# Kernel tuning notes

Measured on AMD Instinct MI355X. Metric: run time of the kernel, lower is better.

Reference implementation:

```python
import jax, jax.numpy as jnp
import numpy as np

HEADS = 4

def _topk_mask(attn, k):
    # exact replica of mask.scatter_(-1, topk_indices, 1.0): exactly k ones per row
    C = attn.shape[-1]
    _, idx = jax.lax.top_k(attn, k)                      # [b,h,C,k]
    return jax.nn.one_hot(idx, C, dtype=attn.dtype).sum(axis=-2) > 0  # [b,h,C,C] bool


def setup_inputs() -> dict:
    key = jax.random.key(0)
    ks = jax.random.split(key, 8)
    b, dim, h, w = 32, 128, 4096, 1
    s = 0.05
    return {
        "x": jax.random.normal(ks[0], (b, dim, h, w), jnp.float32),
        "qkv_w": jax.random.normal(ks[1], (3 * dim, dim), jnp.float32) * s,
        "qkv_b": jax.random.normal(ks[2], (3 * dim,), jnp.float32) * s,
        "dw_w": jax.random.normal(ks[3], (3 * dim, 1, 3, 3), jnp.float32) * s,
        "dw_b": jax.random.normal(ks[4], (3 * dim,), jnp.float32) * s,
        "proj_w": jax.random.normal(ks[5], (dim, dim), jnp.float32) * s,
        "proj_b": jax.random.normal(ks[6], (dim,), jnp.float32) * s,
        "temperature": jnp.ones((HEADS, 1, 1), jnp.float32),
        "attn_w": jnp.full((4,), 0.2, jnp.float32),  # attn1..attn4
    }


def reference(x, qkv_w, qkv_b, dw_w, dw_b, proj_w, proj_b, temperature, attn_w):
    b, c, h, w = x.shape
    # 1x1 conv qkv, then 3x3 depthwise conv (groups = 3*c)
    qkv = jnp.einsum('bchw,oc->bohw', x, qkv_w) + qkv_b[None, :, None, None]
    qkv = jax.lax.conv_general_dilated(
        qkv, dw_w, window_strides=(1, 1), padding=((1, 1), (1, 1)),
        dimension_numbers=('NCHW', 'OIHW', 'NCHW'), feature_group_count=3 * c
    ) + dw_b[None, :, None, None]
    q, k, v = jnp.split(qkv, 3, axis=1)
    heads = lambda t: t.reshape(b, HEADS, c // HEADS, h * w)  # b head c (hw)
    q, k, v = heads(q), heads(k), heads(v)
    # F.normalize(dim=-1), eps=1e-12
    q = q / jnp.maximum(jnp.linalg.norm(q, axis=-1, keepdims=True), 1e-12)
    k = k / jnp.maximum(jnp.linalg.norm(k, axis=-1, keepdims=True), 1e-12)
    C = c // HEADS
    attn = jnp.einsum('bhcn,bhdn->bhcd', q, k) * temperature[None]  # [b,head,C,C]
    top_ks = [C // 2, (2 * C) // 3, (3 * C) // 4, (4 * C) // 5]
    out = jnp.zeros_like(v)
    for i, kk in enumerate(top_ks):
        m = _topk_mask(attn, kk)
        a = jax.nn.softmax(jnp.where(m, attn, -jnp.inf), axis=-1)
        out = out + attn_w[i] * jnp.einsum('bhcd,bhdn->bhcn', a, v)
    out = out.reshape(b, c, h, w)
    out = jnp.einsum('bchw,oc->bohw', out, proj_w) + proj_b[None, :, None, None]
    return out
```

## Files before the change

kernel.cpp:

```cpp
#include <hip/hip_runtime.h>

#define B_ 32
#define CD 128
#define O3 384
#define N  4096
#define H_ 4
#define C_ 32

typedef __bf16 bf16x8 __attribute__((ext_vector_type(8)));
typedef float floatx4 __attribute__((ext_vector_type(4)));

#define MFMA16(a, b, c) __builtin_amdgcn_mfma_f32_16x16x32_bf16(a, b, c, 0, 0, 0)

__device__ __forceinline__ float b2f(unsigned int u) {
  return __builtin_bit_cast(float, u << 16);
}
__device__ __forceinline__ float b2fh(unsigned int u) {
  return __builtin_bit_cast(float, u & 0xffff0000u);
}
__device__ __forceinline__ unsigned short f2b(float f) {
  unsigned int bits = __builtin_bit_cast(unsigned int, f);
  unsigned int r = (bits + 0x7FFFu + ((bits >> 16) & 1u)) >> 16;
  return (unsigned short)r;
}

__global__ __launch_bounds__(256) void k0_xt(const float* __restrict__ x,
                                             unsigned short* __restrict__ xT)
{
  __shared__ float xt[32 * 66];
  const int t = threadIdx.x;
  const int n0 = blockIdx.x * 64, c0 = blockIdx.y * 32, b = blockIdx.z;
  const float* xb = x + ((size_t)b * CD + c0) * N + n0;
#pragma unroll
  for (int i = 0; i < 2; i++) {
    int f = i * 256 + t;
    int c = f >> 4, n4 = (f & 15) * 4;
    float4 v = *(const float4*)(xb + (size_t)c * N + n4);
    *(float2*)&xt[c * 66 + n4]     = make_float2(v.x, v.y);
    *(float2*)&xt[c * 66 + n4 + 2] = make_float2(v.z, v.w);
  }
  __syncthreads();
  int n = t >> 2, cb = (t & 3) * 8;
  unsigned short tmp[8];
#pragma unroll
  for (int j = 0; j < 8; j++) tmp[j] = f2b(xt[(cb + j) * 66 + n]);
  *(uint4*)(xT + ((size_t)b * N + n0 + n) * CD + c0 + cb) = *(uint4*)tmp;
}

__global__ void k0_w(const float* __restrict__ qkv_w,
                     const float* __restrict__ proj_w,
                     const float* __restrict__ dw_w,
                     const float* __restrict__ dw_b,
                     unsigned short* __restrict__ qkv_wb,
                     unsigned short* __restrict__ proj_wb,
                     float4* __restrict__ dwq)
{
  int e = (blockIdx.x * 256 + threadIdx.x) * 4;
  if (e < 49152) {
    float4 v = *(const float4*)(qkv_w + e);
    unsigned short tmp[4] = {f2b(v.x), f2b(v.y), f2b(v.z), f2b(v.w)};
    *(uint2*)(qkv_wb + e) = *(uint2*)tmp;
  } else if (e < 65536) {
    int off = e - 49152;
    float4 v = *(const float4*)(proj_w + off);
    unsigned short tmp[4] = {f2b(v.x), f2b(v.y), f2b(v.z), f2b(v.w)};
    *(uint2*)(proj_wb + off) = *(uint2*)tmp;
  } else {
    int o = (e - 65536) >> 2;
    if (o < 384)
      dwq[o] = make_float4(dw_w[o * 9 + 1], dw_w[o * 9 + 4],
                           dw_w[o * 9 + 7], dw_b[o]);
  }
}

__global__ __launch_bounds__(256, 4) void k1_qkv_dw(
    const unsigned short* __restrict__ xT, const unsigned short* __restrict__ qkv_wb,
    const float* __restrict__ qkv_b, const float4* __restrict__ dwq,
    unsigned short* __restrict__ qkvd, unsigned short* __restrict__ vT)
{
  __shared__ __align__(16) char smem[34816];
  unsigned short* Bs   = (unsigned short*)smem;
  unsigned short* pres = (unsigned short*)smem;

  const int t = threadIdx.x;
  const int otile = blockIdx.x, ytile = blockIdx.y, b = blockIdx.z;
  const int obase = otile * 128;
  const int ybase = ytile * 124;
  const int wv = t >> 6, l = t & 63, quad = l >> 4, lm = l & 15;

  const unsigned short* wbase =
      qkv_wb + (size_t)(obase + wv * 32 + lm) * CD + quad * 8;
  bf16x8 wa0[4], wa1[4];
#pragma unroll
  for (int ks = 0; ks < 4; ks++) {
    wa0[ks] = *(const bf16x8*)(wbase + ks * 32);
    wa1[ks] = *(const bf16x8*)(wbase + 16 * CD + ks * 32);
  }

  if (ytile >= 1 && ytile <= 32) {
#pragma unroll
    for (int i = 0; i < 8; i++) {
      int f = i * 256 + t;
      int row = f >> 4, c8 = (f & 15) * 8;
      *(uint4*)&Bs[row * 136 + c8] =
          *(const uint4*)(xT + ((size_t)b * N + ybase - 2 + row) * CD + c8);
    }
  } else {
#pragma unroll
    for (int i = 0; i < 8; i++) {
      int f = i * 256 + t;
      int row = f >> 4, c8 = (f & 15) * 8;
      int yg = ybase - 2 + row;
      uint4 v = make_uint4(0u, 0u, 0u, 0u);
      if (yg >= 0 && yg < N)
        v = *(const uint4*)(xT + ((size_t)b * N + yg) * CD + c8);
      *(uint4*)&Bs[row * 136 + c8] = v;
    }
  }
  __syncthreads();

  floatx4 acc[2][8];
#pragma unroll
  for (int mt = 0; mt < 2; mt++)
#pragma unroll
    for (int nt = 0; nt < 8; nt++) acc[mt][nt] = (floatx4){0.f, 0.f, 0.f, 0.f};

#pragma unroll
  for (int ks = 0; ks < 4; ks++) {
#pragma unroll
    for (int nt = 0; nt < 8; nt++) {
      bf16x8 bb = *(const bf16x8*)&Bs[(nt * 16 + lm) * 136 + ks * 32 + quad * 8];
      acc[0][nt] = MFMA16(wa0[ks], bb, acc[0][nt]);
      acc[1][nt] = MFMA16(wa1[ks], bb, acc[1][nt]);
    }
  }

  if (otile < 2) {
    __syncthreads();
#pragma unroll
    for (int mt = 0; mt < 2; mt++)
#pragma unroll
      for (int r = 0; r < 4; r++) {
        int o = wv * 32 + mt * 16 + quad * 4 + r;
        float bias = qkv_b[obase + o];
#pragma unroll
        for (int nt = 0; nt < 8; nt++) {
          int i = nt * 16 + lm;
          if (i >= 1) {
            int yg = ybase - 2 + i;
            pres[o * 132 + (i - 1)] =
                f2b((yg >= 0 && yg < N) ? (acc[mt][nt][r] + bias) : 0.f);
          }
        }
      }
    __syncthreads();
    const int p = t & 63, og = t >> 6;
    const bool ok = (p < 62) && (ybase + 2 * p < N);
    const unsigned int* presu = (const unsigned int*)pres;
    for (int r2 = 0; r2 < 32; r2++) {
      int oo = __builtin_amdgcn_readfirstlane(obase + og * 32 + r2);
      float4 wq = dwq[oo];
      int o = oo - obase;
      unsigned int u0 = presu[(o * 132 >> 1) + p];
      unsigned int u1 = presu[(o * 132 >> 1) + p + 1];
      float v0 = b2f(u0), v1 = b2fh(u0), v2 = b2f(u1), v3 = b2fh(u1);
      float out0 = wq.x * v0 + wq.y * v1 + wq.z * v2 + wq.w;
      float out1 = wq.x * v1 + wq.y * v2 + wq.z * v3 + wq.w;
      unsigned int pk = (unsigned int)f2b(out0) |
                        ((unsigned int)f2b(out1) << 16);
      if (ok)
        *(unsigned int*)(qkvd + ((size_t)b * 256 + oo) * N + ybase + 2 * p) = pk;
    }
  } else {
    const int o = t & 127, half = t >> 7;
    const int oo = obase + o;
    const float4 wq = dwq[oo];
    __syncthreads();
#pragma unroll
    for (int mt = 0; mt < 2; mt++)
#pragma unroll
      for (int r = 0; r < 4; r++) {
        int o2 = wv * 32 + mt * 16 + quad * 4 + r;
        float bias = qkv_b[obase + o2];
#pragma unroll
        for (int nt = 0; nt < 8; nt++) {
          int i = nt * 16 + lm;
          int yg = ybase - 2 + i;
          pres[i * 132 + o2] =
              f2b((yg >= 0 && yg < N) ? (acc[mt][nt][r] + bias) : 0.f);
        }
      }
    __syncthreads();
    int i0 = 2 + half * 62;
    float pm = b2f((unsigned int)pres[(i0 - 1) * 132 + o]);
    float pc = b2f((unsigned int)pres[i0 * 132 + o]);
    for (int i = i0; i < i0 + 62; i++) {
      float pp = b2f((unsigned int)pres[(i + 1) * 132 + o]);
      int yo = ybase - 2 + i;
      if (yo < N) {
        float v = wq.x * pm + wq.y * pc + wq.z * pp + wq.w;
        vT[((size_t)b * N + yo) * CD + o] = f2b(v);
      }
      pm = pc; pc = pp;
    }
  }
}

__global__ __launch_bounds__(256, 4) void k3_gram(
    const unsigned short* __restrict__ qkvd, float* __restrict__ part)
{
  __shared__ float red[4 * 8 * 272];
  const int ns = blockIdx.x, h = blockIdx.y, b = blockIdx.z;
  const int t = threadIdx.x;
  const int wv = t >> 6, l = t & 63, quad = l >> 4, lm = l & 15;
  const unsigned short* qb = qkvd + ((size_t)b * 256 + h * C_) * N;
  const unsigned short* kb = qkvd + ((size_t)b * 256 + 128 + h * C_) * N;

  floatx4 acc[8];
#pragma unroll
  for (int i = 0; i < 8; i++) acc[i] = (floatx4){0.f, 0.f, 0.f, 0.f};

  const int nbase = ns * 1024 + wv * 32 + quad * 8;
#pragma unroll
  for (int ch = 0; ch < 8; ch++) {
    int nc = nbase + ch * 128;
    bf16x8 a0 = *(const bf16x8*)(qb + (size_t)lm * N + nc);
    bf16x8 a1 = *(const bf16x8*)(qb + (size_t)(16 + lm) * N + nc);
    bf16x8 b0 = *(const bf16x8*)(kb + (size_t)lm * N + nc);
    bf16x8 b1 = *(const bf16x8*)(kb + (size_t)(16 + lm) * N + nc);
    acc[0] = MFMA16(a0, b0, acc[0]);
    acc[1] = MFMA16(a0, b1, acc[1]);
    acc[2] = MFMA16(a1, b0, acc[2]);
    acc[3] = MFMA16(a1, b1, acc[3]);
    acc[4] = MFMA16(a0, a0, acc[4]);
    acc[5] = MFMA16(a1, a1, acc[5]);
    acc[6] = MFMA16(b0, b0, acc[6]);
    acc[7] = MFMA16(b1, b1, acc[7]);
  }

#pragma unroll
  for (int tl = 0; tl < 8; tl++)
#pragma unroll
    for (int r = 0; r < 4; r++)
      red[wv * 2176 + tl * 272 + (quad * 4 + r) * 17 + lm] = acc[tl][r];
  __syncthreads();

  float* pb = part + ((size_t)(b * H_ + h) * 4 + ns) * 2048;
  for (int e = t; e < 2048; e += 256) {
    int tl = e >> 8, rc = e & 255, row = rc >> 4, col = rc & 15;
    int a = tl * 272 + row * 17 + col;
    float s = red[a] + red[2176 + a] + red[2 * 2176 + a] + red[3 * 2176 + a];
    if (tl < 4) {
      int mt = tl >> 1, nt = tl & 1;
      pb[(mt * 16 + row) * 32 + nt * 16 + col] = s;
    } else if (row == col) {
      if (tl < 6) pb[1024 + (tl - 4) * 16 + row] = s;
      else        pb[1056 + (tl - 6) * 16 + row] = s;
    }
  }
}

__global__ __launch_bounds__(256) void k45(
    const float* __restrict__ part, const unsigned short* __restrict__ proj_wb,
    const float* __restrict__ temperature, const float* __restrict__ attn_w,
    unsigned short* __restrict__ Mb)
{
  __shared__ float La[H_][C_][33];
  __shared__ float sq2[256];
  __shared__ float rn[256];
  __shared__ float exL[H_][C_][33];
  __shared__ unsigned char rkL[H_][C_][C_];
  __shared__ unsigned short AwtT[H_][C_][40];
  const int b = blockIdx.x, t = threadIdx.x;

  const float* pbb = part + (size_t)b * 32768;
  for (int e = t; e < 4 * 2048; e += 256) {
    int h = e >> 11, idx = e & 2047;
    if (idx < 1088) {
      const float* p = pbb + h * 8192 + idx;
      float s = p[0] + p[2048] + p[2 * 2048] + p[3 * 2048];
      if (idx < 1024) La[h][idx >> 5][idx & 31] = s;
      else if (idx < 1056) sq2[h * 32 + (idx - 1024)] = s;
      else sq2[128 + h * 32 + (idx - 1056)] = s;
    }
  }
  __syncthreads();
  rn[t] = 1.f / fmaxf(sqrtf(sq2[t]), 1e-12f);
  __syncthreads();
  for (int e = t; e < 4096; e += 256) {
    int h = e >> 10, i = (e >> 5) & 31, j = e & 31;
    La[h][i][j] *= rn[h * 32 + i] * rn[128 + h * 32 + j] * temperature[h];
  }
  __syncthreads();

  if (t < 128) {
    int h = t >> 5, i = t & 31;
    float m = -1e30f;
    for (int j = 0; j < 32; j++) m = fmaxf(m, La[h][i][j]);
    float S0 = 0.f, S1 = 0.f, S2 = 0.f, S3 = 0.f;
    for (int j = 0; j < 32; j++) {
      float vj = La[h][i][j];
      int r = 0;
      for (int j2 = 0; j2 < 32; j2++) {
        float v2 = La[h][i][j2];
        r += (v2 > vj) || (v2 == vj && j2 < j);
      }
      float e = __expf(vj - m);
      exL[h][i][j] = e;
      rkL[h][i][j] = (unsigned char)r;
      if (r < 16) S0 += e;
      if (r < 21) S1 += e;
      if (r < 24) S2 += e;
      if (r < 25) S3 += e;
    }
    float w0 = attn_w[0] / S0, w1 = attn_w[1] / S1;
    float w2 = attn_w[2] / S2, w3 = attn_w[3] / S3;
    for (int j = 0; j < 32; j++) {
      int r = rkL[h][i][j];
      float cmb = (r < 16 ? w0 : 0.f) + (r < 21 ? w1 : 0.f) +
                  (r < 24 ? w2 : 0.f) + (r < 25 ? w3 : 0.f);
      AwtT[h][j][i] = f2b(exL[h][i][j] * cmb);
    }
  }
  __syncthreads();

  {
    const int wv = t >> 6, l = t & 63, quad = l >> 4, lm = l & 15;
    const int h = wv;
    bf16x8 bfr[2];
#pragma unroll
    for (int jt = 0; jt < 2; jt++)
      bfr[jt] = *(const bf16x8*)&AwtT[h][jt * 16 + lm][quad * 8];
#pragma unroll
    for (int mt = 0; mt < 8; mt++) {
      bf16x8 a = *(const bf16x8*)(proj_wb +
                    (size_t)(mt * 16 + lm) * CD + h * C_ + quad * 8);
#pragma unroll
      for (int jt = 0; jt < 2; jt++) {
        floatx4 acc = (floatx4){0.f, 0.f, 0.f, 0.f};
        acc = MFMA16(a, bfr[jt], acc);
#pragma unroll
        for (int r = 0; r < 4; r++) {
          int row = quad * 4 + r;
          Mb[(size_t)b * 16384 + (mt * 16 + row) * CD + h * C_ + jt * 16 + lm] =
              f2b(acc[r]);
        }
      }
    }
  }
}

__global__ __launch_bounds__(256, 4) void k6_out(
    const unsigned short* __restrict__ vT, const unsigned short* __restrict__ Mb,
    const float* __restrict__ proj_b, float* __restrict__ out)
{
  __shared__ unsigned short Bs[128 * 136];
  const int t = threadIdx.x;
  const int y0 = blockIdx.x * 128, b = blockIdx.y;
  const int wv = t >> 6, l = t & 63, quad = l >> 4, lm = l & 15;

#pragma unroll
  for (int i = 0; i < 8; i++) {
    int f = i * 256 + t;
    int row = f >> 4, c8 = (f & 15) * 8;
    *(uint4*)&Bs[row * 136 + c8] =
        *(const uint4*)(vT + ((size_t)b * N + y0 + row) * CD + c8);
  }
  __syncthreads();

  floatx4 acc[2][8];
#pragma unroll
  for (int mt = 0; mt < 2; mt++)
#pragma unroll
    for (int nt = 0; nt < 8; nt++) acc[mt][nt] = (floatx4){0.f, 0.f, 0.f, 0.f};

  const unsigned short* mbase =
      Mb + (size_t)b * 16384 + (size_t)(wv * 32 + lm) * CD + quad * 8;
#pragma unroll
  for (int ks = 0; ks < 4; ks++) {
    bf16x8 a0 = *(const bf16x8*)(mbase + ks * 32);
    bf16x8 a1 = *(const bf16x8*)(mbase + 16 * CD + ks * 32);
#pragma unroll
    for (int nt = 0; nt < 8; nt++) {
      bf16x8 bb = *(const bf16x8*)&Bs[(nt * 16 + lm) * 136 + ks * 32 + quad * 8];
      acc[0][nt] = MFMA16(a0, bb, acc[0][nt]);
      acc[1][nt] = MFMA16(a1, bb, acc[1][nt]);
    }
  }

#pragma unroll
  for (int mt = 0; mt < 2; mt++)
#pragma unroll
    for (int r = 0; r < 4; r++) {
      int o = wv * 32 + mt * 16 + quad * 4 + r;
      float pb = proj_b[o];
#pragma unroll
      for (int nt = 0; nt < 8; nt++) {
        int y = y0 + nt * 16 + lm;
        out[((size_t)b * CD + o) * N + y] = acc[mt][nt][r] + pb;
      }
    }
}

extern "C" void kernel_launch(void* const* d_in, const int* in_sizes, int n_in,
                              void* d_out, int out_size, void* d_ws, size_t ws_size,
                              hipStream_t stream)
{
  (void)in_sizes; (void)n_in; (void)out_size; (void)ws_size;
  const float* x           = (const float*)d_in[0];
  const float* qkv_w       = (const float*)d_in[1];
  const float* qkv_b       = (const float*)d_in[2];
  const float* dw_w        = (const float*)d_in[3];
  const float* dw_b        = (const float*)d_in[4];
  const float* proj_w      = (const float*)d_in[5];
  const float* proj_b      = (const float*)d_in[6];
  const float* temperature = (const float*)d_in[7];
  const float* attn_w      = (const float*)d_in[8];
  float* out = (float*)d_out;

  unsigned short* xT      = (unsigned short*)d_ws;
  unsigned short* qkv_wb  = xT + (size_t)16777216;
  unsigned short* proj_wb = qkv_wb + 49152;
  unsigned short* qkvd    = proj_wb + 16384;
  unsigned short* vT      = qkvd + (size_t)33554432;
  unsigned short* Mb      = vT + (size_t)16777216;
  float* part = (float*)(Mb + 524288);
  float4* dwq = (float4*)Mb;

  k0_xt    <<<dim3(64, 4, 32),  256, 0, stream>>>(x, xT);
  k0_w     <<<dim3(66),         256, 0, stream>>>(qkv_w, proj_w, dw_w, dw_b,
                                                  qkv_wb, proj_wb, dwq);
  k1_qkv_dw<<<dim3(3, 34, 32),  256, 0, stream>>>(xT, qkv_wb, qkv_b, dwq,
                                                  qkvd, vT);
  k3_gram  <<<dim3(4, H_, B_),  256, 0, stream>>>(qkvd, part);
  k45      <<<dim3(B_),         256, 0, stream>>>(part, proj_wb, temperature,
                                                  attn_w, Mb);
  k6_out   <<<dim3(32, B_),     256, 0, stream>>>(vT, Mb, proj_b, out);
}
```

Before: 255.5 us.

## Fuse weight prep into transpose and softmax stage into gram via last-block counter

Folds the weight-conversion kernel into the x-transpose kernel and merges the per-batch softmax/projection kernel into the gram kernel, where the last of 16 blocks per batch (detected with an atomic counter kept in the output buffer) does the reduction. It also splits interior and border tiles in the qkv/depthwise kernel to drop bounds checks, and vectorizes vT stores to two channels per thread. This removes two launches and the gaps between them. In exchange the gram kernel needs more shared memory at lower occupancy and adds threadfence/atomic ordering.

```diff
diff --git a/kernel.cpp b/kernel.cpp
--- a/kernel.cpp
+++ b/kernel.cpp
@@ -24,10 +24,14 @@
   return (unsigned short)r;
 }
 
-__global__ __launch_bounds__(256) void k0_xt(const float* __restrict__ x,
-                                             unsigned short* __restrict__ xT)
+__global__ __launch_bounds__(256) void k0_xt(
+    const float* __restrict__ x, unsigned short* __restrict__ xT,
+    const float* __restrict__ qkv_w, const float* __restrict__ proj_w,
+    const float* __restrict__ dw_w, const float* __restrict__ dw_b,
+    unsigned short* __restrict__ qkv_wb, unsigned short* __restrict__ proj_wb,
+    float4* __restrict__ dwq, unsigned int* __restrict__ cnt)
 {
-  __shared__ float xt[32 * 66];
+  __shared__ float xt[32 * 68];
   const int t = threadIdx.x;
   const int n0 = blockIdx.x * 64, c0 = blockIdx.y * 32, b = blockIdx.z;
   const float* xb = x + ((size_t)b * CD + c0) * N + n0;
@@ -36,41 +40,39 @@
     int f = i * 256 + t;
     int c = f >> 4, n4 = (f & 15) * 4;
     float4 v = *(const float4*)(xb + (size_t)c * N + n4);
-    *(float2*)&xt[c * 66 + n4]     = make_float2(v.x, v.y);
-    *(float2*)&xt[c * 66 + n4 + 2] = make_float2(v.z, v.w);
-  }
+    *(float4*)&xt[c * 68 + n4] = v;
+  }
+
+  if (blockIdx.z == 0 && blockIdx.y < 2) {
+    int wid = blockIdx.y * 64 + blockIdx.x;
+    if (wid < 66) {
+      int e = (wid * 256 + t) * 4;
+      if (e < 49152) {
+        float4 v = *(const float4*)(qkv_w + e);
+        unsigned short tmp[4] = {f2b(v.x), f2b(v.y), f2b(v.z), f2b(v.w)};
+        *(uint2*)(qkv_wb + e) = *(uint2*)tmp;
+      } else if (e < 65536) {
+        int off = e - 49152;
+        float4 v = *(const float4*)(proj_w + off);
+        unsigned short tmp[4] = {f2b(v.x), f2b(v.y), f2b(v.z), f2b(v.w)};
+        *(uint2*)(proj_wb + off) = *(uint2*)tmp;
+      } else {
+        int o = (e - 65536) >> 2;
+        if (o < 384)
+          dwq[o] = make_float4(dw_w[o * 9 + 1], dw_w[o * 9 + 4],
+                               dw_w[o * 9 + 7], dw_b[o]);
+      }
+    } else if (wid == 66 && t < 32) {
+      cnt[t] = 0u;
+    }
+  }
+
   __syncthreads();
   int n = t >> 2, cb = (t & 3) * 8;
   unsigned short tmp[8];
 #pragma unroll
-  for (int j = 0; j < 8; j++) tmp[j] = f2b(xt[(cb + j) * 66 + n]);
+  for (int j = 0; j < 8; j++) tmp[j] = f2b(xt[(cb + j) * 68 + n]);
   *(uint4*)(xT + ((size_t)b * N + n0 + n) * CD + c0 + cb) = *(uint4*)tmp;
-}
-
-__global__ void k0_w(const float* __restrict__ qkv_w,
-                     const float* __restrict__ proj_w,
-                     const float* __restrict__ dw_w,
-                     const float* __restrict__ dw_b,
-                     unsigned short* __restrict__ qkv_wb,
-                     unsigned short* __restrict__ proj_wb,
-                     float4* __restrict__ dwq)
-{
-  int e = (blockIdx.x * 256 + threadIdx.x) * 4;
-  if (e < 49152) {
-    float4 v = *(const float4*)(qkv_w + e);
-    unsigned short tmp[4] = {f2b(v.x), f2b(v.y), f2b(v.z), f2b(v.w)};
-    *(uint2*)(qkv_wb + e) = *(uint2*)tmp;
-  } else if (e < 65536) {
-    int off = e - 49152;
-    float4 v = *(const float4*)(proj_w + off);
-    unsigned short tmp[4] = {f2b(v.x), f2b(v.y), f2b(v.z), f2b(v.w)};
-    *(uint2*)(proj_wb + off) = *(uint2*)tmp;
-  } else {
-    int o = (e - 65536) >> 2;
-    if (o < 384)
-      dwq[o] = make_float4(dw_w[o * 9 + 1], dw_w[o * 9 + 4],
-                           dw_w[o * 9 + 7], dw_b[o]);
-  }
 }
 
 __global__ __launch_bounds__(256, 4) void k1_qkv_dw(
@@ -87,6 +89,7 @@
   const int obase = otile * 128;
   const int ybase = ytile * 124;
   const int wv = t >> 6, l = t & 63, quad = l >> 4, lm = l & 15;
+  const bool interior = (ytile >= 1 && ytile <= 32);
 
   const unsigned short* wbase =
       qkv_wb + (size_t)(obase + wv * 32 + lm) * CD + quad * 8;
@@ -97,7 +100,7 @@
     wa1[ks] = *(const bf16x8*)(wbase + 16 * CD + ks * 32);
   }
 
-  if (ytile >= 1 && ytile <= 32) {
+  if (interior) {
 #pragma unroll
     for (int i = 0; i < 8; i++) {
       int f = i * 256 + t;
@@ -137,22 +140,37 @@
 
   if (otile < 2) {
     __syncthreads();
-#pragma unroll
-    for (int mt = 0; mt < 2; mt++)
-#pragma unroll
-      for (int r = 0; r < 4; r++) {
-        int o = wv * 32 + mt * 16 + quad * 4 + r;
-        float bias = qkv_b[obase + o];
-#pragma unroll
-        for (int nt = 0; nt < 8; nt++) {
-          int i = nt * 16 + lm;
-          if (i >= 1) {
-            int yg = ybase - 2 + i;
-            pres[o * 132 + (i - 1)] =
-                f2b((yg >= 0 && yg < N) ? (acc[mt][nt][r] + bias) : 0.f);
+    if (interior) {
+#pragma unroll
+      for (int mt = 0; mt < 2; mt++)
+#pragma unroll
+        for (int r = 0; r < 4; r++) {
+          int o = wv * 32 + mt * 16 + quad * 4 + r;
+          float bias = qkv_b[obase + o];
+#pragma unroll
+          for (int nt = 0; nt < 8; nt++) {
+            int i = nt * 16 + lm;
+            if (i >= 1) pres[o * 132 + (i - 1)] = f2b(acc[mt][nt][r] + bias);
           }
         }
-      }
+    } else {
+#pragma unroll
+      for (int mt = 0; mt < 2; mt++)
+#pragma unroll
+        for (int r = 0; r < 4; r++) {
+          int o = wv * 32 + mt * 16 + quad * 4 + r;
+          float bias = qkv_b[obase + o];
+#pragma unroll
+          for (int nt = 0; nt < 8; nt++) {
+            int i = nt * 16 + lm;
+            if (i >= 1) {
+              int yg = ybase - 2 + i;
+              pres[o * 132 + (i - 1)] =
+                  f2b((yg >= 0 && yg < N) ? (acc[mt][nt][r] + bias) : 0.f);
+            }
+          }
+        }
+    }
     __syncthreads();
     const int p = t & 63, og = t >> 6;
     const bool ok = (p < 62) && (ybase + 2 * p < N);
@@ -161,8 +179,8 @@
       int oo = __builtin_amdgcn_readfirstlane(obase + og * 32 + r2);
       float4 wq = dwq[oo];
       int o = oo - obase;
-      unsigned int u0 = presu[(o * 132 >> 1) + p];
-      unsigned int u1 = presu[(o * 132 >> 1) + p + 1];
+      unsigned int u0 = presu[o * 66 + p];
+      unsigned int u1 = presu[o * 66 + p + 1];
       float v0 = b2f(u0), v1 = b2fh(u0), v2 = b2f(u1), v3 = b2fh(u1);
       float out0 = wq.x * v0 + wq.y * v1 + wq.z * v2 + wq.w;
       float out1 = wq.x * v1 + wq.y * v2 + wq.z * v3 + wq.w;
@@ -172,44 +190,80 @@
         *(unsigned int*)(qkvd + ((size_t)b * 256 + oo) * N + ybase + 2 * p) = pk;
     }
   } else {
-    const int o = t & 127, half = t >> 7;
-    const int oo = obase + o;
-    const float4 wq = dwq[oo];
+    const int op = t & 63, quarter = t >> 6;
+    const int o0 = 2 * op;
+    const float4 wqa = dwq[256 + o0];
+    const float4 wqb = dwq[256 + o0 + 1];
     __syncthreads();
-#pragma unroll
-    for (int mt = 0; mt < 2; mt++)
-#pragma unroll
-      for (int r = 0; r < 4; r++) {
-        int o2 = wv * 32 + mt * 16 + quad * 4 + r;
-        float bias = qkv_b[obase + o2];
-#pragma unroll
-        for (int nt = 0; nt < 8; nt++) {
-          int i = nt * 16 + lm;
-          int yg = ybase - 2 + i;
-          pres[i * 132 + o2] =
-              f2b((yg >= 0 && yg < N) ? (acc[mt][nt][r] + bias) : 0.f);
+    if (interior) {
+#pragma unroll
+      for (int mt = 0; mt < 2; mt++)
+#pragma unroll
+        for (int r = 0; r < 4; r++) {
+          int o2 = wv * 32 + mt * 16 + quad * 4 + r;
+          float bias = qkv_b[obase + o2];
+#pragma unroll
+          for (int nt = 0; nt < 8; nt++) {
+            int i = nt * 16 + lm;
+            pres[i * 132 + o2] = f2b(acc[mt][nt][r] + bias);
+          }
         }
+    } else {
+#pragma unroll
+      for (int mt = 0; mt < 2; mt++)
+#pragma unroll
+        for (int r = 0; r < 4; r++) {
+          int o2 = wv * 32 + mt * 16 + quad * 4 + r;
+          float bias = qkv_b[obase + o2];
+#pragma unroll
+          for (int nt = 0; nt < 8; nt++) {
+            int i = nt * 16 + lm;
+            int yg = ybase - 2 + i;
+            pres[i * 132 + o2] =
+                f2b((yg >= 0 && yg < N) ? (acc[mt][nt][r] + bias) : 0.f);
+          }
+        }
+    }
+    __syncthreads();
+    const unsigned int* pu = (const unsigned int*)pres;
+    int i0 = 2 + quarter * 31;
+    unsigned int pm = pu[(i0 - 1) * 66 + op];
+    unsigned int pc = pu[i0 * 66 + op];
+    if (interior) {
+      for (int i = i0; i < i0 + 31; i++) {
+        unsigned int pp = pu[(i + 1) * 66 + op];
+        int yo = ybase - 2 + i;
+        float a0 = wqa.x * b2f(pm) + wqa.y * b2f(pc) + wqa.z * b2f(pp) + wqa.w;
+        float a1 = wqb.x * b2fh(pm) + wqb.y * b2fh(pc) + wqb.z * b2fh(pp) + wqb.w;
+        unsigned int pk = (unsigned int)f2b(a0) | ((unsigned int)f2b(a1) << 16);
+        *(unsigned int*)(vT + ((size_t)b * N + yo) * CD + o0) = pk;
+        pm = pc; pc = pp;
       }
-    __syncthreads();
-    int i0 = 2 + half * 62;
-    float pm = b2f((unsigned int)pres[(i0 - 1) * 132 + o]);
-    float pc = b2f((unsigned int)pres[i0 * 132 + o]);
-    for (int i = i0; i < i0 + 62; i++) {
-      float pp = b2f((unsigned int)pres[(i + 1) * 132 + o]);
-      int yo = ybase - 2 + i;
-      if (yo < N) {
-        float v = wq.x * pm + wq.y * pc + wq.z * pp + wq.w;
-        vT[((size_t)b * N + yo) * CD + o] = f2b(v);
+    } else {
+      for (int i = i0; i < i0 + 31; i++) {
+        unsigned int pp = pu[(i + 1) * 66 + op];
+        int yo = ybase - 2 + i;
+        if (yo >= 0 && yo < N) {
+          float a0 = wqa.x * b2f(pm) + wqa.y * b2f(pc) + wqa.z * b2f(pp) + wqa.w;
+          float a1 = wqb.x * b2fh(pm) + wqb.y * b2fh(pc) + wqb.z * b2fh(pp) + wqb.w;
+          unsigned int pk = (unsigned int)f2b(a0) | ((unsigned int)f2b(a1) << 16);
+          *(unsigned int*)(vT + ((size_t)b * N + yo) * CD + o0) = pk;
+        }
+        pm = pc; pc = pp;
       }
-      pm = pc; pc = pp;
-    }
-  }
-}
-
-__global__ __launch_bounds__(256, 4) void k3_gram(
-    const unsigned short* __restrict__ qkvd, float* __restrict__ part)
+    }
+  }
+}
+
+__global__ __launch_bounds__(256, 2) void k3_gram(
+    const unsigned short* __restrict__ qkvd, float* __restrict__ part,
+    const unsigned short* __restrict__ proj_wb,
+    const float* __restrict__ temperature, const float* __restrict__ attn_w,
+    unsigned short* __restrict__ Mb, unsigned int* __restrict__ cnt)
 {
-  __shared__ float red[4 * 8 * 272];
+  __shared__ __align__(16) char sm[50176];
+  __shared__ int isLast;
+  float* red = (float*)sm;
   const int ns = blockIdx.x, h = blockIdx.y, b = blockIdx.z;
   const int t = threadIdx.x;
   const int wv = t >> 6, l = t & 63, quad = l >> 4, lm = l & 15;
@@ -258,56 +312,60 @@
       else        pb[1056 + (tl - 6) * 16 + row] = s;
     }
   }
-}
-
-__global__ __launch_bounds__(256) void k45(
-    const float* __restrict__ part, const unsigned short* __restrict__ proj_wb,
-    const float* __restrict__ temperature, const float* __restrict__ attn_w,
-    unsigned short* __restrict__ Mb)
-{
-  __shared__ float La[H_][C_][33];
-  __shared__ float sq2[256];
-  __shared__ float rn[256];
-  __shared__ float exL[H_][C_][33];
-  __shared__ unsigned char rkL[H_][C_][C_];
-  __shared__ unsigned short AwtT[H_][C_][40];
-  const int b = blockIdx.x, t = threadIdx.x;
+
+  __threadfence();
+  __syncthreads();
+  if (t == 0) isLast = (atomicAdd(&cnt[b], 1u) == 15u);
+  __syncthreads();
+  if (!isLast) return;
+  __threadfence();
+
+  float* LaF          = (float*)sm;
+  float* sq2          = (float*)(sm + 16896);
+  float* rn           = (float*)(sm + 17920);
+  float* exL          = (float*)(sm + 18944);
+  unsigned char* rkL  = (unsigned char*)(sm + 35840);
+  unsigned short* Aw  = (unsigned short*)(sm + 39936);
+#define LA(hh, ii, jj) LaF[((hh) * C_ + (ii)) * 33 + (jj)]
+#define EXL(hh, ii, jj) exL[((hh) * C_ + (ii)) * 33 + (jj)]
+#define RKL(hh, ii, jj) rkL[((hh) * C_ + (ii)) * C_ + (jj)]
+#define AWT(hh, jj, ii) Aw[((hh) * C_ + (jj)) * 40 + (ii)]
 
   const float* pbb = part + (size_t)b * 32768;
   for (int e = t; e < 4 * 2048; e += 256) {
-    int h = e >> 11, idx = e & 2047;
+    int hh = e >> 11, idx = e & 2047;
     if (idx < 1088) {
-      const float* p = pbb + h * 8192 + idx;
+      const float* p = pbb + hh * 8192 + idx;
       float s = p[0] + p[2048] + p[2 * 2048] + p[3 * 2048];
-      if (idx < 1024) La[h][idx >> 5][idx & 31] = s;
-      else if (idx < 1056) sq2[h * 32 + (idx - 1024)] = s;
-      else sq2[128 + h * 32 + (idx - 1056)] = s;
+      if (idx < 1024) LA(hh, idx >> 5, idx & 31) = s;
+      else if (idx < 1056) sq2[hh * 32 + (idx - 1024)] = s;
+      else sq2[128 + hh * 32 + (idx - 1056)] = s;
     }
   }
   __syncthreads();
   rn[t] = 1.f / fmaxf(sqrtf(sq2[t]), 1e-12f);
   __syncthreads();
   for (int e = t; e < 4096; e += 256) {
-    int h = e >> 10, i = (e >> 5) & 31, j = e & 31;
-    La[h][i][j] *= rn[h * 32 + i] * rn[128 + h * 32 + j] * temperature[h];
+    int hh = e >> 10, i = (e >> 5) & 31, j = e & 31;
+    LA(hh, i, j) *= rn[hh * 32 + i] * rn[128 + hh * 32 + j] * temperature[hh];
   }
   __syncthreads();
 
   if (t < 128) {
-    int h = t >> 5, i = t & 31;
+    int hh = t >> 5, i = t & 31;
     float m = -1e30f;
-    for (int j = 0; j < 32; j++) m = fmaxf(m, La[h][i][j]);
+    for (int j = 0; j < 32; j++) m = fmaxf(m, LA(hh, i, j));
     float S0 = 0.f, S1 = 0.f, S2 = 0.f, S3 = 0.f;
     for (int j = 0; j < 32; j++) {
-      float vj = La[h][i][j];
+      float vj = LA(hh, i, j);
       int r = 0;
       for (int j2 = 0; j2 < 32; j2++) {
-        float v2 = La[h][i][j2];
+        float v2 = LA(hh, i, j2);
         r += (v2 > vj) || (v2 == vj && j2 < j);
       }
       float e = __expf(vj - m);
-      exL[h][i][j] = e;
-      rkL[h][i][j] = (unsigned char)r;
+      EXL(hh, i, j) = e;
+      RKL(hh, i, j) = (unsigned char)r;
       if (r < 16) S0 += e;
       if (r < 21) S1 += e;
       if (r < 24) S2 += e;
@@ -316,38 +374,41 @@
     float w0 = attn_w[0] / S0, w1 = attn_w[1] / S1;
     float w2 = attn_w[2] / S2, w3 = attn_w[3] / S3;
     for (int j = 0; j < 32; j++) {
-      int r = rkL[h][i][j];
+      int r = RKL(hh, i, j);
       float cmb = (r < 16 ? w0 : 0.f) + (r < 21 ? w1 : 0.f) +
                   (r < 24 ? w2 : 0.f) + (r < 25 ? w3 : 0.f);
-      AwtT[h][j][i] = f2b(exL[h][i][j] * cmb);
+      AWT(hh, j, i) = f2b(EXL(hh, i, j) * cmb);
     }
   }
   __syncthreads();
 
   {
-    const int wv = t >> 6, l = t & 63, quad = l >> 4, lm = l & 15;
-    const int h = wv;
+    const int hh = wv;
     bf16x8 bfr[2];
 #pragma unroll
     for (int jt = 0; jt < 2; jt++)
-      bfr[jt] = *(const bf16x8*)&AwtT[h][jt * 16 + lm][quad * 8];
+      bfr[jt] = *(const bf16x8*)&AWT(hh, jt * 16 + lm, quad * 8);
 #pragma unroll
     for (int mt = 0; mt < 8; mt++) {
       bf16x8 a = *(const bf16x8*)(proj_wb +
-                    (size_t)(mt * 16 + lm) * CD + h * C_ + quad * 8);
+                    (size_t)(mt * 16 + lm) * CD + hh * C_ + quad * 8);
 #pragma unroll
       for (int jt = 0; jt < 2; jt++) {
-        floatx4 acc = (floatx4){0.f, 0.f, 0.f, 0.f};
-        acc = MFMA16(a, bfr[jt], acc);
+        floatx4 ac = (floatx4){0.f, 0.f, 0.f, 0.f};
+        ac = MFMA16(a, bfr[jt], ac);
 #pragma unroll
         for (int r = 0; r < 4; r++) {
           int row = quad * 4 + r;
-          Mb[(size_t)b * 16384 + (mt * 16 + row) * CD + h * C_ + jt * 16 + lm] =
-              f2b(acc[r]);
+          Mb[(size_t)b * 16384 + (mt * 16 + row) * CD + hh * C_ + jt * 16 + lm] =
+              f2b(ac[r]);
         }
       }
     }
   }
+#undef LA
+#undef EXL
+#undef RKL
+#undef AWT
 }
 
 __global__ __launch_bounds__(256, 4) void k6_out(
@@ -426,14 +487,14 @@
   unsigned short* Mb      = vT + (size_t)16777216;
   float* part = (float*)(Mb + 524288);
   float4* dwq = (float4*)Mb;
-
-  k0_xt    <<<dim3(64, 4, 32),  256, 0, stream>>>(x, xT);
-  k0_w     <<<dim3(66),         256, 0, stream>>>(qkv_w, proj_w, dw_w, dw_b,
-                                                  qkv_wb, proj_wb, dwq);
+  unsigned int* cnt = (unsigned int*)d_out;
+
+  k0_xt    <<<dim3(64, 4, 32),  256, 0, stream>>>(x, xT, qkv_w, proj_w, dw_w,
+                                                  dw_b, qkv_wb, proj_wb, dwq,
+                                                  cnt);
   k1_qkv_dw<<<dim3(3, 34, 32),  256, 0, stream>>>(xT, qkv_wb, qkv_b, dwq,
                                                   qkvd, vT);
-  k3_gram  <<<dim3(4, H_, B_),  256, 0, stream>>>(qkvd, part);
-  k45      <<<dim3(B_),         256, 0, stream>>>(part, proj_wb, temperature,
-                                                  attn_w, Mb);
+  k3_gram  <<<dim3(4, H_, B_),  256, 0, stream>>>(qkvd, part, proj_wb,
+                                                  temperature, attn_w, Mb, cnt);
   k6_out   <<<dim3(32, B_),     256, 0, stream>>>(vT, Mb, proj_b, out);
 }
```

After: 312.1 us. +22.2%, slower.
